# Kernel optimization log

Hardware: AMD Instinct MI355X
Metric: run time of the kernel (lower is better)

Reference implementation:

```python
import jax, jax.numpy as jnp
import numpy as np


def _lstm_cell(x, h, c, W_ih, W_hh, b_ih, b_hh):
    # torch.nn.LSTMCell math; gate order i, f, g, o
    gates = x @ W_ih.T + b_ih + h @ W_hh.T + b_hh
    i, f, g, o = jnp.split(gates, 4, axis=-1)
    c_new = jax.nn.sigmoid(f) * c + jax.nn.sigmoid(i) * jnp.tanh(g)
    h_new = jax.nn.sigmoid(o) * jnp.tanh(c_new)
    return h_new, c_new


def setup_inputs() -> dict:
    key = jax.random.key(0)
    ks = jax.random.split(key, 14)
    B, T, F = 16384, 128, 12
    H1, H2 = 64, 128
    s0 = 1.0 / np.sqrt(H1)
    s1 = 1.0 / np.sqrt(H2)
    u = lambda k, shape, s: jax.random.uniform(k, shape, jnp.float32, -s, s)
    return {
        "input_seq": jax.random.normal(ks[0], (B, T, F), jnp.float32),
        "W_ih0": u(ks[1], (4 * H1, F), s0),
        "W_hh0": u(ks[2], (4 * H1, H1), s0),
        "b_ih0": u(ks[3], (4 * H1,), s0),
        "b_hh0": u(ks[4], (4 * H1,), s0),
        "W_ih1": u(ks[5], (4 * H2, H1), s1),
        "W_hh1": u(ks[6], (4 * H2, H2), s1),
        "b_ih1": u(ks[7], (4 * H2,), s1),
        "b_hh1": u(ks[8], (4 * H2,), s1),
        "W_d1": u(ks[9], (H1, H2), s1),
        "b_d1": u(ks[10], (H1,), s1),
        "W_d2": u(ks[11], (1, H1), s0),
        "b_d2": u(ks[12], (1,), s0),
    }


def reference(input_seq, W_ih0, W_hh0, b_ih0, b_hh0,
              W_ih1, W_hh1, b_ih1, b_hh1,
              W_d1, b_d1, W_d2, b_d2):
    B = input_seq.shape[0]
    H1 = W_hh0.shape[1]
    H2 = W_hh1.shape[1]
    dt = input_seq.dtype
    init = (jnp.zeros((B, H1), dt), jnp.zeros((B, H1), dt),
            jnp.zeros((B, H2), dt), jnp.zeros((B, H2), dt))

    def step(carry, x_t):
        h0, c0, h1, c1 = carry
        h0, c0 = _lstm_cell(x_t, h0, c0, W_ih0, W_hh0, b_ih0, b_hh0)
        # dropout is identity in eval mode
        h1, c1 = _lstm_cell(h0, h1, c1, W_ih1, W_hh1, b_ih1, b_hh1)
        return (h0, c0, h1, c1), None

    xs = jnp.swapaxes(input_seq, 0, 1)  # [T, B, F]
    (h0, c0, h1, c1), _ = jax.lax.scan(step, init, xs)
    pred = (h1 @ W_d1.T + b_d1) @ W_d2.T + b_d2  # [B, 1]
    return pred
```

## Files before the change

### kernel.cpp

```cpp
#include <hip/hip_runtime.h>
#include <hip/hip_fp16.h>


#define T_STEPS 128
#define F_IN    12
#define R       32
#define S0H     136
#define S1H     520

#define WF0_H8  (16*3*64)
#define WF1_H8  (16*12*64)
#define WH_TOTAL_HALVES ((WF0_H8 + WF1_H8)*8)

typedef _Float16 half8 __attribute__((ext_vector_type(8)));
typedef _Float16 half4 __attribute__((ext_vector_type(4)));
typedef float   floatx4  __attribute__((ext_vector_type(4)));
typedef float   floatx16 __attribute__((ext_vector_type(16)));
typedef int     intx4  __attribute__((ext_vector_type(4)));

__device__ __forceinline__ float vexp2(float x){
  float r; asm("v_exp_f32 %0, %1" : "=v"(r) : "v"(x)); return r;
}
__device__ __forceinline__ float vrcp(float x){
  float r; asm("v_rcp_f32 %0, %1" : "=v"(r) : "v"(x)); return r;
}
__device__ __forceinline__ float sigf(float x){
  return vrcp(1.0f + vexp2(-1.4426950408889634f * x));
}
__device__ __forceinline__ float tanhf_(float x){
  return fmaf(2.0f, vrcp(1.0f + vexp2(-2.8853900817779268f * x)), -1.0f);
}

__device__ __forceinline__ float qpx1(float v){
  return __int_as_float(__builtin_amdgcn_update_dpp(
      0, __float_as_int(v), 0xB1 , 0xF, 0xF, true));
}
__device__ __forceinline__ float qpx2(float v){
  return __int_as_float(__builtin_amdgcn_update_dpp(
      0, __float_as_int(v), 0x4E , 0xF, 0xF, true));
}
__device__ __forceinline__ floatx4 qtrans4(floatx4 s, int g){
  float e0 = qpx1(s[1]), e1 = qpx1(s[0]), e2 = qpx1(s[3]), e3 = qpx1(s[2]);
  const bool lo = (g & 1);
  float m0 = lo ? e0   : s[0];
  float m1 = lo ? s[1] : e1;
  float m2 = lo ? e2   : s[2];
  float m3 = lo ? s[3] : e3;
  float f0 = qpx2(m2), f1 = qpx2(m3), f2 = qpx2(m0), f3 = qpx2(m1);
  const bool hi = (g & 2);
  floatx4 d;
  d[0] = hi ? f0 : m0;
  d[1] = hi ? f1 : m1;
  d[2] = hi ? m2 : f2;
  d[3] = hi ? m3 : f3;
  return d;
}

__global__ void prep_kernel(const float* __restrict__ Wih0, const float* __restrict__ Whh0,
                            const float* __restrict__ bih0, const float* __restrict__ bhh0,
                            const float* __restrict__ Wih1, const float* __restrict__ Whh1,
                            const float* __restrict__ bih1, const float* __restrict__ bhh1,
                            _Float16* __restrict__ wh, float* __restrict__ bs) {
  int tid = blockIdx.x * 256 + threadIdx.x;
  if (tid < WF0_H8) {
    int lane = tid & 63; int kt = (tid >> 6) % 3; int ct = tid / (64*3);
    int p = ct*16 + (lane & 15);
    int col = (p & 3)*64 + (p >> 2);
    int kbase = kt*32 + (lane >> 4)*8;
    #pragma unroll
    for (int j = 0; j < 8; ++j) {
      int k = kbase + j; float w = 0.0f;
      if (k < 12) w = Wih0[col*12 + k];
      else if (k < 76) w = Whh0[col*64 + (k-12)];
      wh[tid*8 + j] = (_Float16)w;
    }
  } else if (tid < WF0_H8 + WF1_H8) {
    int t2 = tid - WF0_H8;
    int lane = t2 & 63; int kt = (t2 >> 6) % 12; int ct = t2 / (64*12);
    int p = ct*32 + (lane & 31);
    int col = (p & 3)*128 + (p >> 2);
    int kbase = kt*16 + (lane >> 5)*8;
    #pragma unroll
    for (int j = 0; j < 8; ++j) {
      int k = kbase + j;
      float w = (k < 64) ? Wih1[col*64 + k] : Whh1[col*128 + (k-64)];
      wh[WF0_H8*8 + t2*8 + j] = (_Float16)w;
    }
  } else if (tid < WF0_H8 + WF1_H8 + 768) {
    int t3 = tid - (WF0_H8 + WF1_H8);
    if (t3 < 256) { int col = (t3 & 3)*64 + (t3 >> 2);  bs[t3] = bih0[col] + bhh0[col]; }
    else { int p1 = t3 - 256; int col = (p1 & 3)*128 + (p1 >> 2); bs[t3] = bih1[col] + bhh1[col]; }
  }
}

__global__ __launch_bounds__(512, 1)
void lstm_kernel(const float* __restrict__ x, const _Float16* __restrict__ wh,
                 const float* __restrict__ bs,
                 const float* __restrict__ Wd1, const float* __restrict__ bd1,
                 const float* __restrict__ Wd2, const float* __restrict__ bd2,
                 float* __restrict__ out) {
  __shared__ __align__(16) _Float16 st0[2*R*S0H];
  __shared__ __align__(16) _Float16 st1[R*S1H];
  __shared__ float hbuf[R*132];
  __shared__ float red[R*17];

  const int tid  = threadIdx.x;
  const int w    = tid >> 6;
  const int lane = tid & 63;
  const int l15  = lane & 15;
  const int l31  = lane & 31;
  const int lg   = lane >> 4;
  const int hi5  = lane >> 5;
  const int qg   = lane & 3;
  const int a    = l15 >> 2;
  const int u    = l31 >> 2;
  const int r    = lg*4 + qg;
  const int rowbase = blockIdx.x * R;

  const intx4* whi = (const intx4*)wh;
  intx4 wb0i[2][3];
  #pragma unroll
  for (int i = 0; i < 2; ++i)
    #pragma unroll
    for (int kt = 0; kt < 3; ++kt) wb0i[i][kt] = whi[((2*w+i)*3 + kt)*64 + lane];
  intx4 wb1i[2][12];
  #pragma unroll
  for (int i = 0; i < 2; ++i)
    #pragma unroll
    for (int kt = 0; kt < 12; ++kt) wb1i[i][kt] = whi[WF0_H8 + ((2*w+i)*12 + kt)*64 + lane];
  float b0[2], b1[2];
  #pragma unroll
  for (int i = 0; i < 2; ++i) b0[i] = bs[(2*w+i)*16 + l15];
  #pragma unroll
  for (int i = 0; i < 2; ++i) b1[i] = bs[256 + (2*w+i)*32 + l31];

  float c0s[2][2] = {{0.0f,0.0f},{0.0f,0.0f}};
  float c1s[2][4] = {{0.0f,0.0f,0.0f,0.0f},{0.0f,0.0f,0.0f,0.0f}};

  const int rdA0 = l15*S0H + lg*8;
  const int rdA1 = l31*S1H + hi5*8;
  const int wrH0st0 = r*S0H + 12 + 8*w + a;
  const int wrH0st1 = r*S1H + 8*w + a;
  const int wrH1 = (4*hi5 + qg)*S1H + 16*w + u;

  for (int i = tid; i < (2*R*S0H)/2; i += 512) ((int*)st0)[i] = 0;
  for (int i = tid; i < (R*S1H)/2;   i += 512) ((int*)st1)[i] = 0;
  __syncthreads();
  const int xr = tid / 3, xq = tid % 3;
  if (tid < 96) {
    float4 v0 = *(const float4*)&x[((size_t)(rowbase + xr)*T_STEPS + 0)*F_IN + xq*4];
    float4 v1 = *(const float4*)&x[((size_t)(rowbase + xr)*T_STEPS + 1)*F_IN + xq*4];
    half4 h40 = {(_Float16)v0.x, (_Float16)v0.y, (_Float16)v0.z, (_Float16)v0.w};
    half4 h41 = {(_Float16)v1.x, (_Float16)v1.y, (_Float16)v1.z, (_Float16)v1.w};
    *(half4*)&st0[xr*S0H + xq*4]           = h40;
    *(half4*)&st0[R*S0H + xr*S0H + xq*4]   = h41;
  }
  __syncthreads();

  auto do_A = [&](int tt, int mt){
    const int pr = tt & 1;
    const int rbase = rdA0 + pr*(R*S0H) + mt*(16*S0H);
    floatx4 acc0 = {b0[0], b0[0], b0[0], b0[0]};
    floatx4 acc1 = {b0[1], b0[1], b0[1], b0[1]};
    #pragma unroll
    for (int kt = 0; kt < 3; ++kt) {
      half8 af = *(const half8*)&st0[rbase + kt*32];
      acc0 = __builtin_amdgcn_mfma_f32_16x16x32_f16(af, __builtin_bit_cast(half8, wb0i[0][kt]), acc0, 0, 0, 0);
      acc1 = __builtin_amdgcn_mfma_f32_16x16x32_f16(af, __builtin_bit_cast(half8, wb0i[1][kt]), acc1, 0, 0, 0);
    }
    #pragma unroll
    for (int i = 0; i < 2; ++i) {
      floatx4 d = qtrans4(i ? acc1 : acc0, qg);
      float c = fmaf(sigf(d[1]), c0s[i][mt], sigf(d[0]) * tanhf_(d[2]));
      c0s[i][mt] = c;
      float h0v = sigf(d[3]) * tanhf_(c);
      _Float16 hh = (_Float16)h0v;
      st0[wrH0st0 + (pr^1)*(R*S0H) + mt*(16*S0H) + 4*i] = hh;
      st1[wrH0st1 + mt*(16*S1H) + pr*192 + 4*i]          = hh;
    }
  };

  auto do_C = [&](int tt){
    const int pr = tt & 1;
    const int rbase = rdA1 + pr*192;
    floatx16 acc0, acc1;
    #pragma unroll
    for (int j = 0; j < 16; ++j) { acc0[j] = b1[0]; acc1[j] = b1[1]; }
    #pragma unroll
    for (int kt = 0; kt < 12; ++kt) {
      half8 af = *(const half8*)&st1[rbase + kt*16];
      acc0 = __builtin_amdgcn_mfma_f32_32x32x16_f16(af, __builtin_bit_cast(half8, wb1i[0][kt]), acc0, 0, 0, 0);
      acc1 = __builtin_amdgcn_mfma_f32_32x32x16_f16(af, __builtin_bit_cast(half8, wb1i[1][kt]), acc1, 0, 0, 0);
    }
    const int wbase = wrH1 + (pr ? 64 : 256);
    #pragma unroll
    for (int i = 0; i < 2; ++i) {
      #pragma unroll
      for (int G = 0; G < 4; ++G) {
        floatx4 s;
        if (i) { s[0]=acc1[4*G+0]; s[1]=acc1[4*G+1]; s[2]=acc1[4*G+2]; s[3]=acc1[4*G+3]; }
        else   { s[0]=acc0[4*G+0]; s[1]=acc0[4*G+1]; s[2]=acc0[4*G+2]; s[3]=acc0[4*G+3]; }
        floatx4 d = qtrans4(s, qg);
        float c = fmaf(sigf(d[1]), c1s[i][G], sigf(d[0]) * tanhf_(d[2]));
        c1s[i][G] = c;
        float h1v = sigf(d[3]) * tanhf_(c);
        st1[wbase + G*(8*S1H) + 8*i] = (_Float16)h1v;
        if (tt == T_STEPS - 1) {
          const int row = 8*G + 4*hi5 + qg;
          hbuf[row*132 + 16*w + 8*i + u] = h1v;
        }
      }
    }
  };

  do_A(0, 0); do_A(0, 1);
  __syncthreads();

  for (int t = 0; t < T_STEPS; t += 2) {
    #pragma unroll
    for (int i = 0; i < 2; ++i) {
      #pragma unroll
      for (int kt = 0; kt < 3; ++kt) asm volatile("" : "+v"(wb0i[i][kt]));
      #pragma unroll
      for (int kt = 0; kt < 12; ++kt) asm volatile("" : "+v"(wb1i[i][kt]));
    }
    asm volatile("" : "+v"(b0[0]), "+v"(b0[1]), "+v"(b1[0]), "+v"(b1[1]));

    #pragma unroll
    for (int hl = 0; hl < 2; ++hl) {
      const int tt = t + hl;
      const int pr = hl;
      float4 xv = {0.0f, 0.0f, 0.0f, 0.0f};
      const bool dopre = (tt + 2 < T_STEPS);
      if (tid < 96 && dopre)
        xv = *(const float4*)&x[((size_t)(rowbase + xr)*T_STEPS + (tt+2))*F_IN + xq*4];

      do_C(tt);
      if (tt + 1 < T_STEPS) { do_A(tt+1, 0); do_A(tt+1, 1); }

      if (tid < 96 && dopre) {
        half4 h4 = {(_Float16)xv.x, (_Float16)xv.y, (_Float16)xv.z, (_Float16)xv.w};
        *(half4*)&st0[pr*(R*S0H) + xr*S0H + xq*4] = h4;
      }
      __syncthreads();
    }
  }

  {
    const int hr = tid & 31, jg = tid >> 5;
    float partial = 0.0f;
    #pragma unroll
    for (int jj = 0; jj < 8; ++jj) {
      int j = jg*8 + jj;
      float dacc = bd1[j];
      const float4* wrow = (const float4*)&Wd1[j*128];
      #pragma unroll 8
      for (int k4 = 0; k4 < 32; ++k4) {
        float4 wv = wrow[k4];
        const float4 hv = *(const float4*)&hbuf[hr*132 + k4*4];
        dacc = fmaf(wv.x, hv.x, dacc); dacc = fmaf(wv.y, hv.y, dacc);
        dacc = fmaf(wv.z, hv.z, dacc); dacc = fmaf(wv.w, hv.w, dacc);
      }
      partial = fmaf(Wd2[j], dacc, partial);
    }
    red[hr*17 + jg] = partial;
  }
  __syncthreads();
  if (tid < R) {
    float ssum = bd2[0];
    #pragma unroll
    for (int k = 0; k < 16; ++k) ssum += red[tid*17 + k];
    out[rowbase + tid] = ssum;
  }
}

extern "C" void kernel_launch(void* const* d_in, const int* in_sizes, int n_in,
                              void* d_out, int out_size, void* d_ws, size_t ws_size,
                              hipStream_t stream) {
  const float* x    = (const float*)d_in[0];
  const float* Wih0 = (const float*)d_in[1];
  const float* Whh0 = (const float*)d_in[2];
  const float* bih0 = (const float*)d_in[3];
  const float* bhh0 = (const float*)d_in[4];
  const float* Wih1 = (const float*)d_in[5];
  const float* Whh1 = (const float*)d_in[6];
  const float* bih1 = (const float*)d_in[7];
  const float* bhh1 = (const float*)d_in[8];
  const float* Wd1  = (const float*)d_in[9];
  const float* bd1  = (const float*)d_in[10];
  const float* Wd2  = (const float*)d_in[11];
  const float* bd2  = (const float*)d_in[12];
  float* out = (float*)d_out;

  _Float16* wh  = (_Float16*)d_ws;
  float*    bsv = (float*)((char*)d_ws + (size_t)WH_TOTAL_HALVES * 2);

  prep_kernel<<<63, 256, 0, stream>>>(Wih0, Whh0, bih0, bhh0, Wih1, Whh1, bih1, bhh1, wh, bsv);
  lstm_kernel<<<512, 512, 0, stream>>>(x, wh, bsv, Wd1, bd1, Wd2, bd2, out);
}
```

Before: 840.2 us.

## Swap MFMA operands to drop DPP transposes and fuse LSTM gate math

Swaps the A/B operands of the MFMA calls so each lane's accumulator already holds the four gates of one hidden unit. This removes the DPP quad-transpose shuffles. The gate nonlinearities are fused into one cell routine that shares reciprocals: fewer rcp calls, with c clamped before the tanh. Biases are preloaded as full accumulator vectors in the new layout, and the st1 stride is shrunk. Weight registers are pinned to AGPRs, which frees VGPRs but may add copies if MFMA cannot read AGPR operands directly for A/B.

```diff
diff --git a/kernel.cpp b/kernel.cpp
--- a/kernel.cpp
+++ b/kernel.cpp
@@ -6,7 +6,7 @@
 #define F_IN    12
 #define R       32
 #define S0H     136
-#define S1H     520
+#define S1H     392
 
 #define WF0_H8  (16*3*64)
 #define WF1_H8  (16*12*64)
@@ -24,36 +24,26 @@
 __device__ __forceinline__ float vrcp(float x){
   float r; asm("v_rcp_f32 %0, %1" : "=v"(r) : "v"(x)); return r;
 }
-__device__ __forceinline__ float sigf(float x){
-  return vrcp(1.0f + vexp2(-1.4426950408889634f * x));
-}
-__device__ __forceinline__ float tanhf_(float x){
-  return fmaf(2.0f, vrcp(1.0f + vexp2(-2.8853900817779268f * x)), -1.0f);
-}
-
-__device__ __forceinline__ float qpx1(float v){
-  return __int_as_float(__builtin_amdgcn_update_dpp(
-      0, __float_as_int(v), 0xB1 , 0xF, 0xF, true));
-}
-__device__ __forceinline__ float qpx2(float v){
-  return __int_as_float(__builtin_amdgcn_update_dpp(
-      0, __float_as_int(v), 0x4E , 0xF, 0xF, true));
-}
-__device__ __forceinline__ floatx4 qtrans4(floatx4 s, int g){
-  float e0 = qpx1(s[1]), e1 = qpx1(s[0]), e2 = qpx1(s[3]), e3 = qpx1(s[2]);
-  const bool lo = (g & 1);
-  float m0 = lo ? e0   : s[0];
-  float m1 = lo ? s[1] : e1;
-  float m2 = lo ? e2   : s[2];
-  float m3 = lo ? s[3] : e3;
-  float f0 = qpx2(m2), f1 = qpx2(m3), f2 = qpx2(m0), f3 = qpx2(m1);
-  const bool hi = (g & 2);
-  floatx4 d;
-  d[0] = hi ? f0 : m0;
-  d[1] = hi ? f1 : m1;
-  d[2] = hi ? m2 : f2;
-  d[3] = hi ? m3 : f3;
-  return d;
+
+__device__ __forceinline__ float lstm_cell(float pi, float pf, float pg, float po, float& c){
+  const float NL2E  = -1.4426950408889634f;
+  const float P2L2E =  2.8853900817779268f;
+  float ei = vexp2(NL2E * pi);
+  float ef = vexp2(NL2E * pf);
+  float gp = vexp2(P2L2E * pg);
+  float eo = vexp2(NL2E * po);
+  float A   = 1.0f + ei;
+  float Bf  = 1.0f + ef;
+  float Gp  = 1.0f + gp;
+  float Gm  = gp - 1.0f;
+  float AGp = A * Gp;
+  float num = fmaf(c, AGp, Bf * Gm);
+  float cn  = num * vrcp(Bf * AGp);
+  c = cn;
+  float tcl = fminf(fmaxf(cn, -15.0f), 15.0f);
+  float e2c = vexp2(P2L2E * tcl);
+  float hd  = (1.0f + eo) * (1.0f + e2c);
+  return (e2c - 1.0f) * vrcp(hd);
 }
 
 __global__ void prep_kernel(const float* __restrict__ Wih0, const float* __restrict__ Whh0,
@@ -111,10 +101,6 @@
   const int l31  = lane & 31;
   const int lg   = lane >> 4;
   const int hi5  = lane >> 5;
-  const int qg   = lane & 3;
-  const int a    = l15 >> 2;
-  const int u    = l31 >> 2;
-  const int r    = lg*4 + qg;
   const int rowbase = blockIdx.x * R;
 
   const intx4* whi = (const intx4*)wh;
@@ -128,20 +114,22 @@
   for (int i = 0; i < 2; ++i)
     #pragma unroll
     for (int kt = 0; kt < 12; ++kt) wb1i[i][kt] = whi[WF0_H8 + ((2*w+i)*12 + kt)*64 + lane];
-  float b0[2], b1[2];
-  #pragma unroll
-  for (int i = 0; i < 2; ++i) b0[i] = bs[(2*w+i)*16 + l15];
-  #pragma unroll
-  for (int i = 0; i < 2; ++i) b1[i] = bs[256 + (2*w+i)*32 + l31];
+  floatx4 bias4[2];
+  #pragma unroll
+  for (int i = 0; i < 2; ++i)
+    #pragma unroll
+    for (int j = 0; j < 4; ++j) bias4[i][j] = bs[(2*w+i)*16 + lg*4 + j];
+  floatx16 bias16[2];
+  #pragma unroll
+  for (int i = 0; i < 2; ++i)
+    #pragma unroll
+    for (int reg = 0; reg < 16; ++reg) {
+      int pl = (reg & 3) + 8*(reg >> 2) + 4*hi5;
+      bias16[i][reg] = bs[256 + (2*w+i)*32 + pl];
+    }
 
   float c0s[2][2] = {{0.0f,0.0f},{0.0f,0.0f}};
   float c1s[2][4] = {{0.0f,0.0f,0.0f,0.0f},{0.0f,0.0f,0.0f,0.0f}};
-
-  const int rdA0 = l15*S0H + lg*8;
-  const int rdA1 = l31*S1H + hi5*8;
-  const int wrH0st0 = r*S0H + 12 + 8*w + a;
-  const int wrH0st1 = r*S1H + 8*w + a;
-  const int wrH1 = (4*hi5 + qg)*S1H + 16*w + u;
 
   for (int i = tid; i < (2*R*S0H)/2; i += 512) ((int*)st0)[i] = 0;
   for (int i = tid; i < (R*S1H)/2;   i += 512) ((int*)st1)[i] = 0;
@@ -152,63 +140,54 @@
     float4 v1 = *(const float4*)&x[((size_t)(rowbase + xr)*T_STEPS + 1)*F_IN + xq*4];
     half4 h40 = {(_Float16)v0.x, (_Float16)v0.y, (_Float16)v0.z, (_Float16)v0.w};
     half4 h41 = {(_Float16)v1.x, (_Float16)v1.y, (_Float16)v1.z, (_Float16)v1.w};
-    *(half4*)&st0[xr*S0H + xq*4]           = h40;
-    *(half4*)&st0[R*S0H + xr*S0H + xq*4]   = h41;
+    *(half4*)&st0[xr*S0H + xq*4]         = h40;
+    *(half4*)&st0[R*S0H + xr*S0H + xq*4] = h41;
   }
   __syncthreads();
 
   auto do_A = [&](int tt, int mt){
-    const int pr = tt & 1;
-    const int rbase = rdA0 + pr*(R*S0H) + mt*(16*S0H);
-    floatx4 acc0 = {b0[0], b0[0], b0[0], b0[0]};
-    floatx4 acc1 = {b0[1], b0[1], b0[1], b0[1]};
+    const int prA = tt & 1;
+    const int rb = prA*(R*S0H) + (16*mt + l15)*S0H + lg*8;
+    floatx4 acc0 = bias4[0], acc1 = bias4[1];
     #pragma unroll
     for (int kt = 0; kt < 3; ++kt) {
-      half8 af = *(const half8*)&st0[rbase + kt*32];
-      acc0 = __builtin_amdgcn_mfma_f32_16x16x32_f16(af, __builtin_bit_cast(half8, wb0i[0][kt]), acc0, 0, 0, 0);
-      acc1 = __builtin_amdgcn_mfma_f32_16x16x32_f16(af, __builtin_bit_cast(half8, wb0i[1][kt]), acc1, 0, 0, 0);
+      half8 sf = *(const half8*)&st0[rb + kt*32];
+      acc0 = __builtin_amdgcn_mfma_f32_16x16x32_f16(__builtin_bit_cast(half8, wb0i[0][kt]), sf, acc0, 0, 0, 0);
+      acc1 = __builtin_amdgcn_mfma_f32_16x16x32_f16(__builtin_bit_cast(half8, wb0i[1][kt]), sf, acc1, 0, 0, 0);
     }
     #pragma unroll
     for (int i = 0; i < 2; ++i) {
-      floatx4 d = qtrans4(i ? acc1 : acc0, qg);
-      float c = fmaf(sigf(d[1]), c0s[i][mt], sigf(d[0]) * tanhf_(d[2]));
-      c0s[i][mt] = c;
-      float h0v = sigf(d[3]) * tanhf_(c);
-      _Float16 hh = (_Float16)h0v;
-      st0[wrH0st0 + (pr^1)*(R*S0H) + mt*(16*S0H) + 4*i] = hh;
-      st1[wrH0st1 + mt*(16*S1H) + pr*192 + 4*i]          = hh;
+      floatx4 ac = i ? acc1 : acc0;
+      float h = lstm_cell(ac[0], ac[1], ac[2], ac[3], c0s[i][mt]);
+      _Float16 hh = (_Float16)h;
+      const int hid = 8*w + 4*i + lg;
+      st0[(prA^1)*(R*S0H) + (16*mt+l15)*S0H + 12 + hid] = hh;
+      st1[(16*mt+l15)*S1H + prA*192 + hid]              = hh;
     }
   };
 
   auto do_C = [&](int tt){
     const int pr = tt & 1;
-    const int rbase = rdA1 + pr*192;
-    floatx16 acc0, acc1;
-    #pragma unroll
-    for (int j = 0; j < 16; ++j) { acc0[j] = b1[0]; acc1[j] = b1[1]; }
+    const int rb = l31*S1H + pr*192 + hi5*8;
+    floatx16 acc0 = bias16[0], acc1 = bias16[1];
     #pragma unroll
     for (int kt = 0; kt < 12; ++kt) {
-      half8 af = *(const half8*)&st1[rbase + kt*16];
-      acc0 = __builtin_amdgcn_mfma_f32_32x32x16_f16(af, __builtin_bit_cast(half8, wb1i[0][kt]), acc0, 0, 0, 0);
-      acc1 = __builtin_amdgcn_mfma_f32_32x32x16_f16(af, __builtin_bit_cast(half8, wb1i[1][kt]), acc1, 0, 0, 0);
-    }
-    const int wbase = wrH1 + (pr ? 64 : 256);
+      half8 sf = *(const half8*)&st1[rb + kt*16];
+      acc0 = __builtin_amdgcn_mfma_f32_32x32x16_f16(__builtin_bit_cast(half8, wb1i[0][kt]), sf, acc0, 0, 0, 0);
+      acc1 = __builtin_amdgcn_mfma_f32_32x32x16_f16(__builtin_bit_cast(half8, wb1i[1][kt]), sf, acc1, 0, 0, 0);
+    }
+    const int wbse = l31*S1H + (pr^1)*192 + 64 + 16*w;
     #pragma unroll
     for (int i = 0; i < 2; ++i) {
       #pragma unroll
       for (int G = 0; G < 4; ++G) {
-        floatx4 s;
-        if (i) { s[0]=acc1[4*G+0]; s[1]=acc1[4*G+1]; s[2]=acc1[4*G+2]; s[3]=acc1[4*G+3]; }
-        else   { s[0]=acc0[4*G+0]; s[1]=acc0[4*G+1]; s[2]=acc0[4*G+2]; s[3]=acc0[4*G+3]; }
-        floatx4 d = qtrans4(s, qg);
-        float c = fmaf(sigf(d[1]), c1s[i][G], sigf(d[0]) * tanhf_(d[2]));
-        c1s[i][G] = c;
-        float h1v = sigf(d[3]) * tanhf_(c);
-        st1[wbase + G*(8*S1H) + 8*i] = (_Float16)h1v;
-        if (tt == T_STEPS - 1) {
-          const int row = 8*G + 4*hi5 + qg;
-          hbuf[row*132 + 16*w + 8*i + u] = h1v;
-        }
+        floatx4 ac;
+        if (i) { ac[0]=acc1[4*G+0]; ac[1]=acc1[4*G+1]; ac[2]=acc1[4*G+2]; ac[3]=acc1[4*G+3]; }
+        else   { ac[0]=acc0[4*G+0]; ac[1]=acc0[4*G+1]; ac[2]=acc0[4*G+2]; ac[3]=acc0[4*G+3]; }
+        float h = lstm_cell(ac[0], ac[1], ac[2], ac[3], c1s[i][G]);
+        const int hid = 8*i + 2*G + hi5;
+        st1[wbse + hid] = (_Float16)h;
+        if (tt == T_STEPS - 1) hbuf[l31*132 + 16*w + hid] = h;
       }
     }
   };
@@ -220,11 +199,11 @@
     #pragma unroll
     for (int i = 0; i < 2; ++i) {
       #pragma unroll
-      for (int kt = 0; kt < 3; ++kt) asm volatile("" : "+v"(wb0i[i][kt]));
+      for (int kt = 0; kt < 3; ++kt) asm volatile("" : "+a"(wb0i[i][kt]));
       #pragma unroll
-      for (int kt = 0; kt < 12; ++kt) asm volatile("" : "+v"(wb1i[i][kt]));
-    }
-    asm volatile("" : "+v"(b0[0]), "+v"(b0[1]), "+v"(b1[0]), "+v"(b1[1]));
+      for (int kt = 0; kt < 12; ++kt) asm volatile("" : "+a"(wb1i[i][kt]));
+      asm volatile("" : "+v"(bias4[i]), "+v"(bias16[i]));
+    }
 
     #pragma unroll
     for (int hl = 0; hl < 2; ++hl) {
```

After: 763.9 us. 9.1% less time.
